# Kernel tuning notes

Hardware: AMD Instinct MI355X
Metric: run time of the kernel (lower is better)

## Reference

```python
import jax, jax.numpy as jnp
import numpy as np

N_NODES = 50000
N_EDGES = 800000
D = 128


def _gcn_layer(h, src, dst, norm, W, b, n_nodes):
    # h: [N, Din]; linear transform first (PyG GCNConv does x @ W then propagate)
    h = h @ W  # [N, Dout]
    msg = h[src] * norm[:, None]  # gather + per-edge scale, [E+N, Dout]
    out = jax.ops.segment_sum(msg, dst, num_segments=n_nodes)  # scatter-add
    return out + b


def setup_inputs() -> dict:
    key = jax.random.key(0)
    k_x, k_e, k_w1, k_w2 = jax.random.split(key, 4)
    x = jax.random.normal(k_x, (N_NODES, D), dtype=jnp.float32)
    edge_index = jax.random.randint(k_e, (2, N_EDGES), 0, N_NODES, dtype=jnp.int64)
    # Glorot-ish init for GCN weights
    s = 1.0 / np.sqrt(D)
    W1 = jax.random.uniform(k_w1, (D, D), jnp.float32, -s, s)
    W2 = jax.random.uniform(k_w2, (D, D), jnp.float32, -s, s)
    b1 = jnp.zeros((D,), jnp.float32)
    b2 = jnp.zeros((D,), jnp.float32)
    return {"x": x, "edge_index": edge_index, "W1": W1, "b1": b1, "W2": W2, "b2": b2}


def reference(x, edge_index, W1, b1, W2, b2):
    n = x.shape[0]
    loop = jnp.arange(n, dtype=edge_index.dtype)
    # add self-loops (GCNConv default add_self_loops=True)
    src = jnp.concatenate([edge_index[0], loop])
    dst = jnp.concatenate([edge_index[1], loop])
    # symmetric normalization: deg counted at aggregation (dst) side
    deg = jax.ops.segment_sum(jnp.ones_like(src, dtype=x.dtype), dst, num_segments=n)
    dinv = jnp.where(deg > 0, jax.lax.rsqrt(deg), 0.0)
    norm = dinv[src] * dinv[dst]  # [E+N]
    h = jax.nn.relu(_gcn_layer(x, src, dst, norm, W1, b1, n))
    # F.dropout(p=0.2, training=False) -> identity in eval mode
    h = jax.nn.relu(_gcn_layer(h, src, dst, norm, W2, b2, n))
    return h
```

## Files before the change

### kernel.cpp

```cpp
#include <hip/hip_runtime.h>
#include <hip/hip_bf16.h>

typedef __hip_bfloat16 bf16h;
typedef short short8 __attribute__((ext_vector_type(8)));
typedef float floatx4 __attribute__((ext_vector_type(4)));

__device__ __forceinline__ float bfu2f(unsigned int u) {
    return __uint_as_float((u & 0xffffu) << 16);
}
__device__ __forceinline__ float bfhi2f(unsigned int u) {
    return __uint_as_float(u & 0xffff0000u);
}
__device__ __forceinline__ unsigned short f2bfu(float f) {
    bf16h b = __float2bfloat16(f);
    return *(unsigned short*)&b;
}

#define SLOTS 64

__global__ __launch_bounds__(256) void k_prep(const void* __restrict__ x,
                                              const void* __restrict__ W1, const void* __restrict__ b1,
                                              const void* __restrict__ W2, const void* __restrict__ b2,
                                              int* __restrict__ cnt,
                                              unsigned short* __restrict__ W1h, unsigned short* __restrict__ W1l,
                                              unsigned short* __restrict__ W2h, unsigned short* __restrict__ W2l,
                                              float* __restrict__ bfv1, float* __restrict__ bfv2,
                                              unsigned int* __restrict__ Xb, int n) {
    int t = threadIdx.x;
    __shared__ int sIsB;
    if (t < 64) {
        unsigned int w = ((const unsigned int*)x)[t];
        unsigned int ef = (w >> 7) & 0xFFu;
        unsigned long long b = __ballot(ef >= 0x76u && ef <= 0x82u);
        if (t == 0) sIsB = (__popcll(b) >= 40) ? 1 : 0;
    }
    __syncthreads();
    bool isb = sIsB != 0;

    int gsz = gridDim.x * 256;
    int gid = blockIdx.x * 256 + t;
    for (int i = gid; i < n; i += gsz) cnt[i] = 0;
    for (int i = gid; i < 16384; i += gsz) {
        int c  = i >> 11;
        int kk = (i >> 9) & 3;
        int ln = (i >> 3) & 63;
        int j  = i & 7;
        int k    = kk * 32 + (ln >> 4) * 8 + j;
        int ncol = c * 16 + (ln & 15);
        int src  = k * 128 + ncol;
        float v1 = isb ? bfu2f(((const unsigned short*)W1)[src]) : ((const float*)W1)[src];
        float v2 = isb ? bfu2f(((const unsigned short*)W2)[src]) : ((const float*)W2)[src];
        unsigned short h1 = f2bfu(v1), h2 = f2bfu(v2);
        W1h[i] = h1; W1l[i] = f2bfu(v1 - bfu2f(h1));
        W2h[i] = h2; W2l[i] = f2bfu(v2 - bfu2f(h2));
    }
    if (gid < 128) {
        bfv1[gid] = isb ? bfu2f(((const unsigned short*)b1)[gid]) : ((const float*)b1)[gid];
        bfv2[gid] = isb ? bfu2f(((const unsigned short*)b2)[gid]) : ((const float*)b2)[gid];
    }
    int total = n * 64;
    if (isb) {
        const unsigned int* xs = (const unsigned int*)x;
        for (int i = gid; i < total; i += gsz) Xb[i] = xs[i];
    } else {
        const float2* xf = (const float2*)x;
        for (int i = gid; i < total; i += gsz) {
            float2 v = xf[i];
            Xb[i] = ((unsigned int)f2bfu(v.y) << 16) | f2bfu(v.x);
        }
    }
}

__global__ __launch_bounds__(256) void k_countfill(const int* __restrict__ ei,
                                                   int* __restrict__ cnt,
                                                   int* __restrict__ slots,
                                                   int e, int n, int rpx) {
    __shared__ int sSt;
    int t = threadIdx.x;
    if (t < 64) {
        int v = ei[2 * t + 1];
        unsigned long long b = __ballot(v == 0);
        if (t == 0) sSt = (b == ~0ull) ? 2 : 1;
    }
    __syncthreads();
    int st = sSt;
    int xcd = blockIdx.x & 7;
    int i = (blockIdx.x >> 3) * 256 + t;
    if (i >= e) return;
    int d = ei[(size_t)e * st + (size_t)i * st];
    int lo = xcd * rpx, hi = min(n, lo + rpx);
    if (d < lo || d >= hi) return;
    int s = ei[(size_t)i * st];
    if (s < 0 || s >= n) return;
    int pos = atomicAdd(&cnt[d], 1);
    if (pos < SLOTS) slots[(size_t)d * SLOTS + pos] = s;
}

template <bool OUT_BF16>
__global__ __launch_bounds__(256) void k_fused(const unsigned int* __restrict__ Xt,
                                               const int* __restrict__ cnt,
                                               const int* __restrict__ slots,
                                               const unsigned short* __restrict__ Wh,
                                               const unsigned short* __restrict__ Wl,
                                               const float* __restrict__ bias,
                                               void* __restrict__ out, int n) {
    __shared__ float sA[16][132];
    int t = threadIdx.x;
    int wv = t >> 6, lane = t & 63;
    int g = lane >> 4, l = lane & 15;
    int col = l * 4;
    int rowBase = blockIdx.x * 16;
    int nm1 = n - 1;

    for (int r = 0; r < 4; ++r) {
        int i = r * 4 + wv;
        int node = rowBase + i;
        int nodeC = min(node, nm1);
        int deg = (node < n) ? cnt[nodeC] : 0;
        int end = min(deg, SLOTS);
        const int* sl = slots + (size_t)nodeC * SLOTS;
        float acc[8] = {0.f, 0.f, 0.f, 0.f, 0.f, 0.f, 0.f, 0.f};
        for (int j = 0; j < end; j += 16) {
#pragma unroll
            for (int k = 0; k < 4; ++k) {
                int jj = j + k * 4 + g;
                bool ok = jj < end;
                int s = ok ? sl[jj] : nodeC;
                s = min(max(s, 0), nm1);
                float w = ok ? rsqrtf((float)cnt[s] + 1.0f) : 0.f;
                uint4 v = *(const uint4*)(Xt + (size_t)s * 64 + col);
                acc[0] += w * bfu2f(v.x);  acc[1] += w * bfhi2f(v.x);
                acc[2] += w * bfu2f(v.y);  acc[3] += w * bfhi2f(v.y);
                acc[4] += w * bfu2f(v.z);  acc[5] += w * bfhi2f(v.z);
                acc[6] += w * bfu2f(v.w);  acc[7] += w * bfhi2f(v.w);
            }
        }
#pragma unroll
        for (int q = 0; q < 8; ++q) {
            acc[q] += __shfl_xor(acc[q], 16, 64);
            acc[q] += __shfl_xor(acc[q], 32, 64);
        }
        if (g == 0) {
            float wd = rsqrtf((float)deg + 1.0f);
            uint4 v = *(const uint4*)(Xt + (size_t)nodeC * 64 + col);
            acc[0] += wd * bfu2f(v.x);  acc[1] += wd * bfhi2f(v.x);
            acc[2] += wd * bfu2f(v.y);  acc[3] += wd * bfhi2f(v.y);
            acc[4] += wd * bfu2f(v.z);  acc[5] += wd * bfhi2f(v.z);
            acc[6] += wd * bfu2f(v.w);  acc[7] += wd * bfhi2f(v.w);
            float* po = &sA[i][l * 8];
#pragma unroll
            for (int q = 0; q < 8; ++q) po[q] = wd * acc[q];
        }
    }
    __syncthreads();

    floatx4 acc2[2];
    acc2[0] = (floatx4){0.f, 0.f, 0.f, 0.f};
    acc2[1] = (floatx4){0.f, 0.f, 0.f, 0.f};

#pragma unroll
    for (int kk = 0; kk < 4; ++kk) {
        const float* ap = &sA[l][kk * 32 + g * 8];
        float av[8];
#pragma unroll
        for (int j2 = 0; j2 < 8; ++j2) av[j2] = ap[j2];
        short8 ah, alo;
#pragma unroll
        for (int j2 = 0; j2 < 8; ++j2) {
            unsigned short h = f2bfu(av[j2]);
            ah[j2]  = (short)h;
            alo[j2] = (short)f2bfu(av[j2] - bfu2f(h));
        }
#pragma unroll
        for (int cc = 0; cc < 2; ++cc) {
            int c = wv * 2 + cc;
            int fo = ((c * 4 + kk) * 64 + lane) * 8;
            short8 bh = *(const short8*)(Wh + fo);
            short8 bl = *(const short8*)(Wl + fo);
            acc2[cc] = __builtin_amdgcn_mfma_f32_16x16x32_bf16(ah, bh, acc2[cc], 0, 0, 0);
            acc2[cc] = __builtin_amdgcn_mfma_f32_16x16x32_bf16(alo, bh, acc2[cc], 0, 0, 0);
            acc2[cc] = __builtin_amdgcn_mfma_f32_16x16x32_bf16(ah, bl, acc2[cc], 0, 0, 0);
        }
    }

#pragma unroll
    for (int cc = 0; cc < 2; ++cc) {
        int c = wv * 2 + cc;
        int ncol = c * 16 + l;
        float bv = bias[ncol];
#pragma unroll
        for (int r = 0; r < 4; ++r) {
            int row = rowBase + g * 4 + r;
            if (row < n) {
                float o = fmaxf(acc2[cc][r] + bv, 0.f);
                if constexpr (OUT_BF16) {
                    ((unsigned short*)out)[(size_t)row * 128 + ncol] = f2bfu(o);
                } else {
                    ((float*)out)[(size_t)row * 128 + ncol] = o;
                }
            }
        }
    }
}

extern "C" void kernel_launch(void* const* d_in, const int* in_sizes, int n_in,
                              void* d_out, int out_size, void* d_ws, size_t ws_size,
                              hipStream_t stream) {
    const int n = in_sizes[0] / 128;
    const int e = in_sizes[1] / 2;
    const void* x = d_in[0];
    const int* ei = (const int*)d_in[1];

    char* w = (char*)d_ws;
    size_t o = 0;
    auto alloc = [&](size_t bytes) -> char* {
        char* p = w + o;
        o += (bytes + 255) & ~(size_t)255;
        return p;
    };
    int* cnt   = (int*)alloc((size_t)n * 4);
    int* slots = (int*)alloc((size_t)n * SLOTS * 4);
    unsigned short* W1h = (unsigned short*)alloc(16384 * 2);
    unsigned short* W1l = (unsigned short*)alloc(16384 * 2);
    unsigned short* W2h = (unsigned short*)alloc(16384 * 2);
    unsigned short* W2l = (unsigned short*)alloc(16384 * 2);
    float* bf1 = (float*)alloc(128 * 4);
    float* bf2 = (float*)alloc(128 * 4);
    unsigned int* Xb  = (unsigned int*)alloc((size_t)n * 64 * 4);
    unsigned int* Xb2 = (unsigned int*)alloc((size_t)n * 64 * 4);
    (void)ws_size;

    k_prep<<<1024, 256, 0, stream>>>(x, d_in[2], d_in[3], d_in[4], d_in[5],
                                     cnt, W1h, W1l, W2h, W2l, bf1, bf2, Xb, n);
    const int rpx = (n + 7) / 8;
    int ecx = ((e + 255) / 256) * 8;
    k_countfill<<<ecx, 256, 0, stream>>>(ei, cnt, slots, e, n, rpx);

    int gf = (n + 15) / 16;
    k_fused<true><<<gf, 256, 0, stream>>>(Xb, cnt, slots, W1h, W1l, bf1, Xb2, n);
    k_fused<false><<<gf, 256, 0, stream>>>(Xb2, cnt, slots, W2h, W2l, bf2, d_out, n);
}
```

Baseline: 237.7 us.

## Drop XCD-partitioned edge fill and gather one node per 16-lane group

New measurement: 241.7 us. Within noise of the previous version (+1.7%).

```diff
diff --git a/kernel.cpp b/kernel.cpp
--- a/kernel.cpp
+++ b/kernel.cpp
@@ -74,7 +74,7 @@
 __global__ __launch_bounds__(256) void k_countfill(const int* __restrict__ ei,
                                                    int* __restrict__ cnt,
                                                    int* __restrict__ slots,
-                                                   int e, int n, int rpx) {
+                                                   int e, int n) {
     __shared__ int sSt;
     int t = threadIdx.x;
     if (t < 64) {
@@ -84,12 +84,10 @@
     }
     __syncthreads();
     int st = sSt;
-    int xcd = blockIdx.x & 7;
-    int i = (blockIdx.x >> 3) * 256 + t;
+    int i = blockIdx.x * 256 + t;
     if (i >= e) return;
     int d = ei[(size_t)e * st + (size_t)i * st];
-    int lo = xcd * rpx, hi = min(n, lo + rpx);
-    if (d < lo || d >= hi) return;
+    if (d < 0 || d >= n) return;
     int s = ei[(size_t)i * st];
     if (s < 0 || s >= n) return;
     int pos = atomicAdd(&cnt[d], 1);
@@ -112,45 +110,40 @@
     int rowBase = blockIdx.x * 16;
     int nm1 = n - 1;
 
-    for (int r = 0; r < 4; ++r) {
-        int i = r * 4 + wv;
-        int node = rowBase + i;
-        int nodeC = min(node, nm1);
-        int deg = (node < n) ? cnt[nodeC] : 0;
-        int end = min(deg, SLOTS);
-        const int* sl = slots + (size_t)nodeC * SLOTS;
-        float acc[8] = {0.f, 0.f, 0.f, 0.f, 0.f, 0.f, 0.f, 0.f};
-        for (int j = 0; j < end; j += 16) {
-#pragma unroll
-            for (int k = 0; k < 4; ++k) {
-                int jj = j + k * 4 + g;
-                bool ok = jj < end;
-                int s = ok ? sl[jj] : nodeC;
-                s = min(max(s, 0), nm1);
-                float w = ok ? rsqrtf((float)cnt[s] + 1.0f) : 0.f;
-                uint4 v = *(const uint4*)(Xt + (size_t)s * 64 + col);
-                acc[0] += w * bfu2f(v.x);  acc[1] += w * bfhi2f(v.x);
-                acc[2] += w * bfu2f(v.y);  acc[3] += w * bfhi2f(v.y);
-                acc[4] += w * bfu2f(v.z);  acc[5] += w * bfhi2f(v.z);
-                acc[6] += w * bfu2f(v.w);  acc[7] += w * bfhi2f(v.w);
-            }
-        }
-#pragma unroll
-        for (int q = 0; q < 8; ++q) {
-            acc[q] += __shfl_xor(acc[q], 16, 64);
-            acc[q] += __shfl_xor(acc[q], 32, 64);
-        }
-        if (g == 0) {
-            float wd = rsqrtf((float)deg + 1.0f);
-            uint4 v = *(const uint4*)(Xt + (size_t)nodeC * 64 + col);
-            acc[0] += wd * bfu2f(v.x);  acc[1] += wd * bfhi2f(v.x);
-            acc[2] += wd * bfu2f(v.y);  acc[3] += wd * bfhi2f(v.y);
-            acc[4] += wd * bfu2f(v.z);  acc[5] += wd * bfhi2f(v.z);
-            acc[6] += wd * bfu2f(v.w);  acc[7] += wd * bfhi2f(v.w);
-            float* po = &sA[i][l * 8];
-#pragma unroll
-            for (int q = 0; q < 8; ++q) po[q] = wd * acc[q];
-        }
+    int i = wv * 4 + g;
+    int node = rowBase + i;
+    int nodeC = min(node, nm1);
+    int deg = (node < n) ? cnt[nodeC] : 0;
+    int end = min(deg, SLOTS);
+    const int* sl = slots + (size_t)nodeC * SLOTS;
+    float acc[8] = {0.f, 0.f, 0.f, 0.f, 0.f, 0.f, 0.f, 0.f};
+    int4 sv = *(const int4*)(sl);
+    for (int j = 0; j < end; j += 4) {
+        int4 cur = sv;
+        if (j + 4 < end) sv = *(const int4*)(sl + j + 4);
+        int ss[4] = {cur.x, cur.y, cur.z, cur.w};
+#pragma unroll
+        for (int k = 0; k < 4; ++k) {
+            bool ok = (j + k) < end;
+            int s = ok ? ss[k] : nodeC;
+            float w = ok ? rsqrtf((float)cnt[s] + 1.0f) : 0.f;
+            uint4 v = *(const uint4*)(Xt + (size_t)s * 64 + col);
+            acc[0] += w * bfu2f(v.x);  acc[1] += w * bfhi2f(v.x);
+            acc[2] += w * bfu2f(v.y);  acc[3] += w * bfhi2f(v.y);
+            acc[4] += w * bfu2f(v.z);  acc[5] += w * bfhi2f(v.z);
+            acc[6] += w * bfu2f(v.w);  acc[7] += w * bfhi2f(v.w);
+        }
+    }
+    {
+        float wd = rsqrtf((float)deg + 1.0f);
+        uint4 v = *(const uint4*)(Xt + (size_t)nodeC * 64 + col);
+        acc[0] += wd * bfu2f(v.x);  acc[1] += wd * bfhi2f(v.x);
+        acc[2] += wd * bfu2f(v.y);  acc[3] += wd * bfhi2f(v.y);
+        acc[4] += wd * bfu2f(v.z);  acc[5] += wd * bfhi2f(v.z);
+        acc[6] += wd * bfu2f(v.w);  acc[7] += wd * bfhi2f(v.w);
+        float* po = &sA[i][l * 8];
+#pragma unroll
+        for (int q = 0; q < 8; ++q) po[q] = wd * acc[q];
     }
     __syncthreads();
 
@@ -219,7 +212,7 @@
         return p;
     };
     int* cnt   = (int*)alloc((size_t)n * 4);
-    int* slots = (int*)alloc((size_t)n * SLOTS * 4);
+    int* slots = (int*)alloc((size_t)n * SLOTS * 4 + 16);
     unsigned short* W1h = (unsigned short*)alloc(16384 * 2);
     unsigned short* W1l = (unsigned short*)alloc(16384 * 2);
     unsigned short* W2h = (unsigned short*)alloc(16384 * 2);
@@ -232,9 +225,8 @@
 
     k_prep<<<1024, 256, 0, stream>>>(x, d_in[2], d_in[3], d_in[4], d_in[5],
                                      cnt, W1h, W1l, W2h, W2l, bf1, bf2, Xb, n);
-    const int rpx = (n + 7) / 8;
-    int ecx = ((e + 255) / 256) * 8;
-    k_countfill<<<ecx, 256, 0, stream>>>(ei, cnt, slots, e, n, rpx);
+    int eb = (e + 255) / 256;
+    k_countfill<<<eb, 256, 0, stream>>>(ei, cnt, slots, e, n);
 
     int gf = (n + 15) / 16;
     k_fused<true><<<gf, 256, 0, stream>>>(Xb, cnt, slots, W1h, W1l, bf1, Xb2, n);
```
